# Optimization experiments

Hardware: AMD Instinct MI355X
Metric: run time of the kernel (lower is better)

## Reference

```python
import jax, jax.numpy as jnp
import numpy as np

B, S, D, H = 4, 2048, 512, 8
DH = D // H  # depth per head = 64


def setup_inputs() -> dict:
    key = jax.random.key(0)
    ks = jax.random.split(key, 8)
    scale = 1.0 / np.sqrt(D)
    return {
        "query": jax.random.normal(ks[0], (B, S, D), jnp.float32),
        "key": jax.random.normal(ks[1], (B, S, D), jnp.float32),
        "value": jax.random.normal(ks[2], (B, S, D), jnp.float32),
        "mask": jax.random.randint(ks[3], (B, S), 0, 2, jnp.int32),
        "wq_w": jax.random.normal(ks[4], (D, D), jnp.float32) * scale,
        "wq_b": jnp.zeros((D,), jnp.float32),
        "wk_w": jax.random.normal(ks[5], (D, D), jnp.float32) * scale,
        "wk_b": jnp.zeros((D,), jnp.float32),
        "wv_w": jax.random.normal(ks[6], (D, D), jnp.float32) * scale,
        "wv_b": jnp.zeros((D,), jnp.float32),
        "wo_w": jax.random.normal(ks[7], (D, D), jnp.float32) * scale,
        "wo_b": jnp.zeros((D,), jnp.float32),
    }


def _split_heads(x):
    # [B, S, D] -> [B, H, S, DH]
    b, s, _ = x.shape
    return x.reshape(b, s, H, DH).transpose(0, 2, 1, 3)


def reference(query, key, value, mask, wq_w, wq_b, wk_w, wk_b, wv_w, wv_b, wo_w, wo_b):
    q = _split_heads(query @ wq_w + wq_b)   # [B,H,S,DH]
    k = _split_heads(key @ wk_w + wk_b)
    v = _split_heads(value @ wv_w + wv_b)

    scale = 1.0 / jnp.sqrt(jnp.asarray(DH, jnp.float32))
    logits = jnp.einsum('bhqd,bhkd->bhqk', q, k) * scale  # [B,H,S,S]
    # additive key-padding mask: 1 -> masked (adds -1e9)
    m = mask.astype(logits.dtype)[:, None, None, :]  # [B,1,1,S]
    logits = logits + m * -1e9
    weights = jax.nn.softmax(logits, axis=-1)
    attn = jnp.einsum('bhqk,bhkd->bhqd', weights, v)  # [B,H,S,DH]
    attn = attn.transpose(0, 2, 1, 3).reshape(query.shape[0], -1, D)  # [B,S,D]
    return attn @ wo_w + wo_b
```

## Files before the change

kernel.cpp:

```cpp
#include <hip/hip_runtime.h>
#include <stdint.h>

#define QSCALE (0.125f * 1.44269504088896340736f)
#define MASKNEG (-1.442695e9f)

typedef unsigned short u16;
typedef unsigned int u32;
typedef __bf16 bf16x8 __attribute__((ext_vector_type(8)));
typedef float f32x4 __attribute__((ext_vector_type(4)));
typedef u16 u16x8 __attribute__((ext_vector_type(8)));

__device__ __forceinline__ u16 f2bf(float f) {
  u32 u = __float_as_uint(f);
  u += 0x7fffu + ((u >> 16) & 1u);
  return (u16)(u >> 16);
}

__device__ __forceinline__ void gload16(const void* src, void* ldsbase) {
  __builtin_amdgcn_global_load_lds(
      (const __attribute__((address_space(1))) u32*)src,
      (__attribute__((address_space(3))) u32*)ldsbase, 16, 0, 0);
}

__global__ __launch_bounds__(256) void conv_in(const float* __restrict__ q,
                                               const float* __restrict__ k,
                                               const float* __restrict__ v,
                                               u16* __restrict__ dst) {
  const float* src = (blockIdx.z == 0) ? q : (blockIdx.z == 1) ? k : v;
  u16* d = dst + (size_t)blockIdx.z * 4194304;
  size_t i = ((size_t)blockIdx.x * 256 + threadIdx.x) * 8;
  float4 a = *(const float4*)(src + i);
  float4 b = *(const float4*)(src + i + 4);
  u16x8 ov;
  ov[0] = f2bf(a.x); ov[1] = f2bf(a.y); ov[2] = f2bf(a.z); ov[3] = f2bf(a.w);
  ov[4] = f2bf(b.x); ov[5] = f2bf(b.y); ov[6] = f2bf(b.z); ov[7] = f2bf(b.w);
  *(u16x8*)(d + i) = ov;
}

__global__ __launch_bounds__(256) void conv_w(const float* __restrict__ wq,
                                              const float* __restrict__ wk,
                                              const float* __restrict__ wv,
                                              const float* __restrict__ wo,
                                              u16* __restrict__ wT) {
  const float* src = (blockIdx.z == 0) ? wq : (blockIdx.z == 1) ? wk
                    : (blockIdx.z == 2) ? wv : wo;
  u16* dst = wT + (size_t)blockIdx.z * 262144;
  __shared__ float t[64][65];
  const int n0 = blockIdx.x * 64, k0 = blockIdx.y * 64;
  const int lr = threadIdx.x >> 6, lc = threadIdx.x & 63;
#pragma unroll
  for (int it = 0; it < 16; ++it) {
    const int row = it * 4 + lr;
    t[row][lc] = src[(size_t)(k0 + row) * 512 + n0 + lc];
  }
  __syncthreads();
#pragma unroll
  for (int it = 0; it < 16; ++it) {
    const int row = it * 4 + lr;
    dst[(size_t)(n0 + row) * 512 + k0 + lc] = f2bf(t[lc][row]);
  }
}

__device__ __forceinline__ void gemm_core(const u16* __restrict__ A,
                                          const u16* __restrict__ Bt,
                                          int m0, int n0, char* lds,
                                          f32x4 acc[4][4]) {
  const int tid = threadIdx.x;
  const int lane = tid & 63;
  const int wave = tid >> 6;
  const int wm = wave >> 1, wn = wave & 1;
  const int srow = tid >> 3;
  const int sc16 = tid & 7;

  auto stage = [&](int buf, int kt) {
    const int k0 = kt * 64;
    char* base = lds + buf * 32768;
#pragma unroll
    for (int c = 0; c < 4; ++c) {
      const int row = c * 32 + srow;
      const int xc = (sc16 ^ (row & 7)) << 3;
      gload16(A + (size_t)(m0 + row) * 512 + k0 + xc,
              base + c * 4096 + (wave << 10));
      gload16(Bt + (size_t)(n0 + row) * 512 + k0 + xc,
              base + 16384 + c * 4096 + (wave << 10));
    }
  };

  auto compute = [&](int buf) {
    const char* bA = lds + buf * 32768;
    const char* bB = bA + 16384;
#pragma unroll
    for (int kk = 0; kk < 2; ++kk) {
      const int c16 = kk * 4 + (lane >> 4);
      bf16x8 av[4], bv[4];
#pragma unroll
      for (int i = 0; i < 4; ++i) {
        const int row = wm * 64 + i * 16 + (lane & 15);
        av[i] = *(const bf16x8*)(bA + row * 128 + ((c16 ^ (row & 7)) << 4));
      }
#pragma unroll
      for (int j = 0; j < 4; ++j) {
        const int row = wn * 64 + j * 16 + (lane & 15);
        bv[j] = *(const bf16x8*)(bB + row * 128 + ((c16 ^ (row & 7)) << 4));
      }
#pragma unroll
      for (int i = 0; i < 4; ++i)
#pragma unroll
        for (int j = 0; j < 4; ++j)
          acc[i][j] = __builtin_amdgcn_mfma_f32_16x16x32_bf16(av[i], bv[j],
                                                              acc[i][j], 0, 0, 0);
    }
  };

  stage(0, 0);
  __syncthreads();
#pragma unroll
  for (int kt = 0; kt < 8; ++kt) {
    const int cur = kt & 1;
    if (kt < 7) stage(cur ^ 1, kt + 1);
    compute(cur);
    __syncthreads();
  }
}

__global__ __launch_bounds__(256) void gemm_qkv(
    const u16* __restrict__ xq, const u16* __restrict__ xk,
    const u16* __restrict__ xv, const u16* __restrict__ wT,
    const float* __restrict__ bq, const float* __restrict__ bk,
    const float* __restrict__ bv, u16* __restrict__ qws, u16* __restrict__ kws,
    u16* __restrict__ vTw) {
  __shared__ __align__(16) char lds[65536];
  const int z = blockIdx.z;
  const u16* A = (z == 0) ? xq : (z == 1) ? xk : xv;
  const u16* Bt = wT + (size_t)z * 262144;
  const float* bias = (z == 0) ? bq : (z == 1) ? bk : bv;
  const int m0 = blockIdx.y * 128, n0 = blockIdx.x * 128;
  f32x4 acc[4][4] = {};
  gemm_core(A, Bt, m0, n0, lds, acc);
  const int lane = threadIdx.x & 63, wave = threadIdx.x >> 6;
  const int wm = wave >> 1, wn = wave & 1;
#pragma unroll
  for (int j = 0; j < 4; ++j) {
    const int n = n0 + wn * 64 + j * 16 + (lane & 15);
    const float bn = bias[n];
    const int h = n >> 6, dh = n & 63;
#pragma unroll
    for (int i = 0; i < 4; ++i) {
#pragma unroll
      for (int r = 0; r < 4; ++r) {
        const int rg = m0 + wm * 64 + i * 16 + ((lane >> 4) << 2) + r;
        const int b = rg >> 11, s = rg & 2047;
        const int bh = b * 8 + h;
        const float val = acc[i][j][r] + bn;
        if (z == 0) {
          qws[((size_t)bh * 2048 + s) * 64 + dh] = f2bf(val * QSCALE);
        } else if (z == 1) {
          kws[((size_t)bh * 2048 + s) * 64 + dh] = f2bf(val);
        } else {
          vTw[((size_t)bh * 64 + dh) * 2048 + s] = f2bf(val);
        }
      }
    }
  }
}

__global__ __launch_bounds__(512) void attn_fwd(const u16* __restrict__ qws,
                                                const u16* __restrict__ kws,
                                                const u16* __restrict__ vTw,
                                                const int* __restrict__ mask,
                                                u16* __restrict__ attn) {
  __shared__ __align__(16) char ldsK[32768];
  __shared__ __align__(16) char ldsV[32768];
  __shared__ __align__(16) char plds[16384];
  const int qt = blockIdx.x;
  const int bh = blockIdx.y;
  const int b = bh >> 3;
  const int tid = threadIdx.x;
  const int lane = tid & 63, wave = tid >> 6;
  const int half = wave >> 2, wl = wave & 3;

  const u16* qbase = qws + ((size_t)bh * 2048 + qt * 64 + wl * 16) * 64;
  bf16x8 qa[2];
#pragma unroll
  for (int kk = 0; kk < 2; ++kk)
    qa[kk] = *(const bf16x8*)(qbase + (lane & 15) * 64 + kk * 32 + (lane >> 4) * 8);

  char* myK = ldsK + half * 16384;
  char* myV = ldsV + half * 16384;
  const int srow = wl * 8 + (lane >> 3);
  const int sc16 = lane & 7;

  auto stage = [&](int buf, int ktg) {
#pragma unroll
    for (int c = 0; c < 2; ++c) {
      const int row = c * 32 + srow;
      const int xc = (sc16 ^ (row & 7)) << 3;
      gload16(kws + ((size_t)bh * 2048 + ktg * 64 + row) * 64 + xc,
              myK + buf * 8192 + c * 4096 + (wl << 10));
      gload16(vTw + ((size_t)bh * 64 + row) * 2048 + ktg * 64 + xc,
              myV + buf * 8192 + c * 4096 + (wl << 10));
    }
  };

  float rs[4] = {};
  f32x4 o[4] = {};
  char* pw = plds + wave * 2048;

  stage(0, half * 16);
  __syncthreads();

  for (int kt = 0; kt < 16; ++kt) {
    const int cur = kt & 1;
    const int ktg = half * 16 + kt;
    float mb[4];
#pragma unroll
    for (int t = 0; t < 4; ++t)
      mb[t] = mask[b * 2048 + ktg * 64 + t * 16 + (lane & 15)] ? MASKNEG : 0.0f;

    if (kt < 15) stage(cur ^ 1, ktg + 1);

    const char* kb = myK + cur * 8192;
    f32x4 sv[4] = {};
    __builtin_amdgcn_s_setprio(1);
#pragma unroll
    for (int t = 0; t < 4; ++t) {
      const int row = t * 16 + (lane & 15);
#pragma unroll
      for (int kk = 0; kk < 2; ++kk) {
        const int c16 = kk * 4 + (lane >> 4);
        const bf16x8 kf =
            *(const bf16x8*)(kb + row * 128 + ((c16 ^ (row & 7)) << 4));
        sv[t] = __builtin_amdgcn_mfma_f32_16x16x32_bf16(qa[kk], kf, sv[t], 0, 0, 0);
      }
    }
    __builtin_amdgcn_s_setprio(0);

#pragma unroll
    for (int t = 0; t < 4; ++t) {
#pragma unroll
      for (int r = 0; r < 4; ++r) {
        const float p = __builtin_amdgcn_exp2f(sv[t][r] + mb[t]);
        rs[r] += p;
        const int prow = ((lane >> 4) << 2) + r;
        const int off =
            prow * 128 + (((t * 32 + (lane & 15) * 2)) ^ ((prow & 7) << 4));
        *(__bf16*)(pw + off) = (__bf16)p;
      }
    }

    const char* vb = myV + cur * 8192;
    __builtin_amdgcn_s_setprio(1);
#pragma unroll
    for (int kk = 0; kk < 2; ++kk) {
      const int arow = lane & 15;
      const bf16x8 pa = *(const bf16x8*)(pw + arow * 128 +
                            ((kk * 64 + (lane >> 4) * 16) ^ ((arow & 7) << 4)));
#pragma unroll
      for (int dt = 0; dt < 4; ++dt) {
        const int vrow = dt * 16 + (lane & 15);
        const int c16 = kk * 4 + (lane >> 4);
        const bf16x8 vf =
            *(const bf16x8*)(vb + vrow * 128 + ((c16 ^ (vrow & 7)) << 4));
        o[dt] = __builtin_amdgcn_mfma_f32_16x16x32_bf16(pa, vf, o[dt], 0, 0, 0);
      }
    }
    __builtin_amdgcn_s_setprio(0);
    __syncthreads();
  }

  float lsum[4];
#pragma unroll
  for (int r = 0; r < 4; ++r) {
    float s = rs[r];
    s += __shfl_xor(s, 1);
    s += __shfl_xor(s, 2);
    s += __shfl_xor(s, 4);
    s += __shfl_xor(s, 8);
    lsum[r] = s;
  }

  float* oSh = (float*)ldsK;
  float* lSh = (float*)ldsV;
  if (half == 1) {
#pragma unroll
    for (int dt = 0; dt < 4; ++dt)
#pragma unroll
      for (int r = 0; r < 4; ++r)
        oSh[wl * 1024 + (((lane >> 4) << 2) + r) * 64 + dt * 16 + (lane & 15)] =
            o[dt][r];
    if ((lane & 15) == 0) {
#pragma unroll
      for (int r = 0; r < 4; ++r)
        lSh[wl * 16 + ((lane >> 4) << 2) + r] = lsum[r];
    }
  }
  __syncthreads();
  if (half == 0) {
    const int h = bh & 7;
    float invl[4];
#pragma unroll
    for (int r = 0; r < 4; ++r)
      invl[r] = 1.0f / (lsum[r] + lSh[wl * 16 + ((lane >> 4) << 2) + r]);
    const int sq0 = qt * 64 + wl * 16 + ((lane >> 4) << 2);
#pragma unroll
    for (int dt = 0; dt < 4; ++dt) {
      const int dcol = h * 64 + dt * 16 + (lane & 15);
#pragma unroll
      for (int r = 0; r < 4; ++r) {
        const float val =
            (o[dt][r] +
             oSh[wl * 1024 + (((lane >> 4) << 2) + r) * 64 + dt * 16 + (lane & 15)]) *
            invl[r];
        attn[(size_t)(b * 2048 + sq0 + r) * 512 + dcol] = f2bf(val);
      }
    }
  }
}

__global__ __launch_bounds__(256) void gemm_out(const u16* __restrict__ attn,
                                                const u16* __restrict__ woT,
                                                const float* __restrict__ bo,
                                                float* __restrict__ out) {
  __shared__ __align__(16) char lds[65536];
  const int m0 = blockIdx.y * 128, n0 = blockIdx.x * 128;
  f32x4 acc[4][4] = {};
  gemm_core(attn, woT, m0, n0, lds, acc);
  const int lane = threadIdx.x & 63, wave = threadIdx.x >> 6;
  const int wm = wave >> 1, wn = wave & 1;
#pragma unroll
  for (int j = 0; j < 4; ++j) {
    const int n = n0 + wn * 64 + j * 16 + (lane & 15);
    const float bn = bo[n];
#pragma unroll
    for (int i = 0; i < 4; ++i) {
      const int rbase = m0 + wm * 64 + i * 16 + ((lane >> 4) << 2);
#pragma unroll
      for (int r = 0; r < 4; ++r)
        out[(size_t)(rbase + r) * 512 + n] = acc[i][j][r] + bn;
    }
  }
}

extern "C" void kernel_launch(void* const* d_in, const int* in_sizes, int n_in,
                              void* d_out, int out_size, void* d_ws,
                              size_t ws_size, hipStream_t stream) {
  (void)in_sizes; (void)n_in; (void)out_size; (void)ws_size;
  const float* q = (const float*)d_in[0];
  const float* k = (const float*)d_in[1];
  const float* v = (const float*)d_in[2];
  const int* mask = (const int*)d_in[3];
  const float* wq = (const float*)d_in[4];
  const float* bq = (const float*)d_in[5];
  const float* wk = (const float*)d_in[6];
  const float* bk = (const float*)d_in[7];
  const float* wv = (const float*)d_in[8];
  const float* bv = (const float*)d_in[9];
  const float* wo = (const float*)d_in[10];
  const float* bo = (const float*)d_in[11];

  u16* xq = (u16*)d_ws;
  u16* xk = xq + 4194304;
  u16* xv = xk + 4194304;
  u16* wT = xv + 4194304;
  u16* qws = wT + 1048576;
  u16* kws = qws + 4194304;
  u16* vTw = kws + 4194304;
  u16* attn = xq;
  float* out = (float*)d_out;

  conv_in<<<dim3(2048, 1, 3), 256, 0, stream>>>(q, k, v, xq);
  conv_w<<<dim3(8, 8, 4), 256, 0, stream>>>(wq, wk, wv, wo, wT);
  gemm_qkv<<<dim3(4, 64, 3), 256, 0, stream>>>(xq, xk, xv, wT, bq, bk, bv, qws,
                                               kws, vTw);
  attn_fwd<<<dim3(32, 32), 512, 0, stream>>>(qws, kws, vTw, mask, attn);
  gemm_out<<<dim3(4, 64), 256, 0, stream>>>(attn, wT + 786432, bo, out);
}
```

Measured before the change: 120.4 us.

## Transpose QK^T MFMA operands to produce S^T and write P with packed stores

Swaps the A/B operands of the QK^T MFMA so each lane holds four consecutive keys for a single query row. P can then be written to LDS as one packed 4-element bf16 store instead of four scalar stores, and the mask is read with one int4 load. The row-sum becomes a single scalar per lane, reduced across lane groups and redistributed with shuffles. It also precomputes the swizzled LDS offsets and adds a min-blocks launch bound of 4 per CU, which may force register spilling.

```diff
diff --git a/kernel.cpp b/kernel.cpp
--- a/kernel.cpp
+++ b/kernel.cpp
@@ -7,6 +7,7 @@
 typedef unsigned short u16;
 typedef unsigned int u32;
 typedef __bf16 bf16x8 __attribute__((ext_vector_type(8)));
+typedef __bf16 bf16x4 __attribute__((ext_vector_type(4)));
 typedef float f32x4 __attribute__((ext_vector_type(4)));
 typedef u16 u16x8 __attribute__((ext_vector_type(8)));
 
@@ -164,11 +165,10 @@
   }
 }
 
-__global__ __launch_bounds__(512) void attn_fwd(const u16* __restrict__ qws,
-                                                const u16* __restrict__ kws,
-                                                const u16* __restrict__ vTw,
-                                                const int* __restrict__ mask,
-                                                u16* __restrict__ attn) {
+__global__ __launch_bounds__(512, 4) void attn_fwd(
+    const u16* __restrict__ qws, const u16* __restrict__ kws,
+    const u16* __restrict__ vTw, const int* __restrict__ mask,
+    u16* __restrict__ attn) {
   __shared__ __align__(16) char ldsK[32768];
   __shared__ __align__(16) char ldsV[32768];
   __shared__ __align__(16) char plds[16384];
@@ -178,12 +178,21 @@
   const int tid = threadIdx.x;
   const int lane = tid & 63, wave = tid >> 6;
   const int half = wave >> 2, wl = wave & 3;
+  const int hi = lane >> 4;
+  const int q15 = lane & 15;
+
+  const int rb = q15 * 128;
+  const int xorb = (lane & 7) << 4;
+  const int kx0 = ((hi) ^ (lane & 7)) << 4;
+  const int kx1 = ((4 + hi) ^ (lane & 7)) << 4;
+  const int px0 = (hi * 16) ^ xorb;
+  const int px1 = (64 + hi * 16) ^ xorb;
 
   const u16* qbase = qws + ((size_t)bh * 2048 + qt * 64 + wl * 16) * 64;
   bf16x8 qa[2];
 #pragma unroll
   for (int kk = 0; kk < 2; ++kk)
-    qa[kk] = *(const bf16x8*)(qbase + (lane & 15) * 64 + kk * 32 + (lane >> 4) * 8);
+    qa[kk] = *(const bf16x8*)(qbase + q15 * 64 + kk * 32 + hi * 8);
 
   char* myK = ldsK + half * 16384;
   char* myV = ldsV + half * 16384;
@@ -202,7 +211,7 @@
     }
   };
 
-  float rs[4] = {};
+  float rs = 0.f;
   f32x4 o[4] = {};
   char* pw = plds + wave * 2048;
 
@@ -212,10 +221,11 @@
   for (int kt = 0; kt < 16; ++kt) {
     const int cur = kt & 1;
     const int ktg = half * 16 + kt;
-    float mb[4];
+
+    int4 mm[4];
 #pragma unroll
     for (int t = 0; t < 4; ++t)
-      mb[t] = mask[b * 2048 + ktg * 64 + t * 16 + (lane & 15)] ? MASKNEG : 0.0f;
+      mm[t] = *(const int4*)(mask + b * 2048 + ktg * 64 + t * 16 + hi * 4);
 
     if (kt < 15) stage(cur ^ 1, ktg + 1);
 
@@ -224,43 +234,36 @@
     __builtin_amdgcn_s_setprio(1);
 #pragma unroll
     for (int t = 0; t < 4; ++t) {
-      const int row = t * 16 + (lane & 15);
-#pragma unroll
-      for (int kk = 0; kk < 2; ++kk) {
-        const int c16 = kk * 4 + (lane >> 4);
-        const bf16x8 kf =
-            *(const bf16x8*)(kb + row * 128 + ((c16 ^ (row & 7)) << 4));
-        sv[t] = __builtin_amdgcn_mfma_f32_16x16x32_bf16(qa[kk], kf, sv[t], 0, 0, 0);
-      }
+      const bf16x8 kf0 = *(const bf16x8*)(kb + t * 2048 + rb + kx0);
+      const bf16x8 kf1 = *(const bf16x8*)(kb + t * 2048 + rb + kx1);
+      sv[t] = __builtin_amdgcn_mfma_f32_16x16x32_bf16(kf0, qa[0], sv[t], 0, 0, 0);
+      sv[t] = __builtin_amdgcn_mfma_f32_16x16x32_bf16(kf1, qa[1], sv[t], 0, 0, 0);
     }
     __builtin_amdgcn_s_setprio(0);
 
 #pragma unroll
     for (int t = 0; t < 4; ++t) {
+      const int mmv[4] = {mm[t].x, mm[t].y, mm[t].z, mm[t].w};
+      bf16x4 pk;
 #pragma unroll
       for (int r = 0; r < 4; ++r) {
-        const float p = __builtin_amdgcn_exp2f(sv[t][r] + mb[t]);
-        rs[r] += p;
-        const int prow = ((lane >> 4) << 2) + r;
-        const int off =
-            prow * 128 + (((t * 32 + (lane & 15) * 2)) ^ ((prow & 7) << 4));
-        *(__bf16*)(pw + off) = (__bf16)p;
-      }
+        const float p =
+            __builtin_amdgcn_exp2f(sv[t][r] + (mmv[r] ? MASKNEG : 0.0f));
+        rs += p;
+        pk[r] = (__bf16)p;
+      }
+      *(bf16x4*)(pw + rb + ((t * 32 + hi * 8) ^ xorb)) = pk;
     }
 
     const char* vb = myV + cur * 8192;
     __builtin_amdgcn_s_setprio(1);
 #pragma unroll
     for (int kk = 0; kk < 2; ++kk) {
-      const int arow = lane & 15;
-      const bf16x8 pa = *(const bf16x8*)(pw + arow * 128 +
-                            ((kk * 64 + (lane >> 4) * 16) ^ ((arow & 7) << 4)));
+      const bf16x8 pa = *(const bf16x8*)(pw + rb + (kk ? px1 : px0));
 #pragma unroll
       for (int dt = 0; dt < 4; ++dt) {
-        const int vrow = dt * 16 + (lane & 15);
-        const int c16 = kk * 4 + (lane >> 4);
         const bf16x8 vf =
-            *(const bf16x8*)(vb + vrow * 128 + ((c16 ^ (vrow & 7)) << 4));
+            *(const bf16x8*)(vb + dt * 2048 + rb + (kk ? kx1 : kx0));
         o[dt] = __builtin_amdgcn_mfma_f32_16x16x32_bf16(pa, vf, o[dt], 0, 0, 0);
       }
     }
@@ -268,16 +271,12 @@
     __syncthreads();
   }
 
-  float lsum[4];
-#pragma unroll
-  for (int r = 0; r < 4; ++r) {
-    float s = rs[r];
-    s += __shfl_xor(s, 1);
-    s += __shfl_xor(s, 2);
-    s += __shfl_xor(s, 4);
-    s += __shfl_xor(s, 8);
-    lsum[r] = s;
-  }
+  float lred = rs;
+  lred += __shfl_xor(lred, 16);
+  lred += __shfl_xor(lred, 32);
+  float lq[4];
+#pragma unroll
+  for (int r = 0; r < 4; ++r) lq[r] = __shfl(lred, hi * 4 + r);
 
   float* oSh = (float*)ldsK;
   float* lSh = (float*)ldsV;
@@ -286,13 +285,8 @@
     for (int dt = 0; dt < 4; ++dt)
 #pragma unroll
       for (int r = 0; r < 4; ++r)
-        oSh[wl * 1024 + (((lane >> 4) << 2) + r) * 64 + dt * 16 + (lane & 15)] =
-            o[dt][r];
-    if ((lane & 15) == 0) {
-#pragma unroll
-      for (int r = 0; r < 4; ++r)
-        lSh[wl * 16 + ((lane >> 4) << 2) + r] = lsum[r];
-    }
+        oSh[wl * 1024 + (hi * 4 + r) * 64 + dt * 16 + q15] = o[dt][r];
+    if (hi == 0) lSh[wl * 16 + q15] = lred;
   }
   __syncthreads();
   if (half == 0) {
@@ -300,16 +294,15 @@
     float invl[4];
 #pragma unroll
     for (int r = 0; r < 4; ++r)
-      invl[r] = 1.0f / (lsum[r] + lSh[wl * 16 + ((lane >> 4) << 2) + r]);
-    const int sq0 = qt * 64 + wl * 16 + ((lane >> 4) << 2);
+      invl[r] = 1.0f / (lq[r] + lSh[wl * 16 + hi * 4 + r]);
+    const int sq0 = qt * 64 + wl * 16 + hi * 4;
 #pragma unroll
     for (int dt = 0; dt < 4; ++dt) {
-      const int dcol = h * 64 + dt * 16 + (lane & 15);
+      const int dcol = h * 64 + dt * 16 + q15;
 #pragma unroll
       for (int r = 0; r < 4; ++r) {
         const float val =
-            (o[dt][r] +
-             oSh[wl * 1024 + (((lane >> 4) << 2) + r) * 64 + dt * 16 + (lane & 15)]) *
+            (o[dt][r] + oSh[wl * 1024 + (hi * 4 + r) * 64 + dt * 16 + q15]) *
             invl[r];
         attn[(size_t)(b * 2048 + sq0 + r) * 512 + dcol] = f2bf(val);
       }
```

Measured after the change: 123.2 us. 1.02x slower.
